# Kernel tuning notes

Hardware: AMD Instinct MI355X
Metric: run time of the kernel (lower is better)

The kernel has to match this reference:

```python
import jax, jax.numpy as jnp
import numpy as np

B, P, IN_DIM, OUT_DIM = 4, 120000, 4, 64
SPATIAL = (480, 360, 32)
EPS = 1e-5
SLOPE = 0.01  # LeakyReLU default negative slope


def setup_inputs() -> dict:
    key = jax.random.key(0)
    ks = jax.random.split(key, 10)
    pc = jax.random.normal(ks[0], (B, P, IN_DIM), dtype=jnp.float32)
    pc_indices = jax.random.randint(ks[1], (B, P, 3), 0, 32, dtype=jnp.int32)
    W1 = jax.random.normal(ks[2], (IN_DIM, 16), dtype=jnp.float32) * (1.0 / np.sqrt(IN_DIM))
    b1 = jax.random.normal(ks[3], (16,), dtype=jnp.float32) * 0.01
    g1 = jnp.ones((16,), jnp.float32)
    be1 = jnp.zeros((16,), jnp.float32)
    W2 = jax.random.normal(ks[4], (16, OUT_DIM), dtype=jnp.float32) * 0.25
    b2 = jax.random.normal(ks[5], (OUT_DIM,), dtype=jnp.float32) * 0.01
    g2 = jnp.ones((OUT_DIM,), jnp.float32)
    be2 = jnp.zeros((OUT_DIM,), jnp.float32)
    return {"pc": pc, "pc_indices": pc_indices, "W1": W1, "b1": b1, "g1": g1,
            "be1": be1, "W2": W2, "b2": b2, "g2": g2, "be2": be2}


def _bn_lrelu(h, g, b):
    # BatchNorm1d in training mode: batch mean / biased variance over points
    mean = jnp.mean(h, axis=0)
    var = jnp.mean((h - mean) ** 2, axis=0)
    h = (h - mean) / jnp.sqrt(var + EPS) * g + b
    return jnp.where(h >= 0, h, SLOPE * h)


def reference(pc, pc_indices, W1, b1, g1, be1, W2, b2, g2, be2):
    N = B * P
    x = pc.reshape(N, IN_DIM)
    bid = jnp.repeat(jnp.arange(B, dtype=jnp.int32), P)  # batch id padded in front
    coords = jnp.concatenate([bid[:, None], pc_indices.reshape(N, 3)], axis=1)  # [N,4]

    # small MLP (shuffle/recover in the original is a mathematical no-op for outputs)
    h = _bn_lrelu(x @ W1 + b1, g1, be1)
    feat = _bn_lrelu(h @ W2 + b2, g2, be2)  # [N, OUT_DIM]

    # torch.unique(dim=0) == lexicographic sort of linearized voxel keys
    S0, S1, S2 = SPATIAL
    key = (((coords[:, 0] * S0 + coords[:, 1]) * S1 + coords[:, 2]) * S2 + coords[:, 3])
    order = jnp.argsort(key)
    sk = key[order]
    is_first = jnp.concatenate([jnp.ones((1,), bool), sk[1:] != sk[:-1]])
    seg_sorted = (jnp.cumsum(is_first) - 1).astype(jnp.int32)  # segment id per sorted point
    inv = jnp.zeros((N,), jnp.int32).at[order].set(seg_sorted)  # inverse index (unsorted)

    # scatter_max into (padded, fixed-shape) voxel feature table
    voxel_feat = jax.ops.segment_max(feat, inv, num_segments=N)  # [N, OUT_DIM]
    n_uni = seg_sorted[-1] + 1
    valid = jnp.arange(N) < n_uni
    voxel_feat = jnp.where(valid[:, None], voxel_feat, 0.0)
    voxel_ind = jnp.zeros((N, 4), jnp.int32).at[seg_sorted].set(coords[order])

    return voxel_feat, voxel_ind, feat
```

## Files before the change

### kernel.cpp

```cpp
#include <hip/hip_runtime.h>

typedef unsigned int u32;
typedef unsigned char u8;

#define N_PTS 480000
#define PPB   120000
#define NKEY  131072
#define NBLK_A 256
#define NBLK_B 512
#define NT64   7500
#define SLOPE 0.01f

__device__ __forceinline__ u32 mapf(float f) {
    u32 u = __float_as_uint(f);
    return (u & 0x80000000u) ? ~u : (u | 0x80000000u);
}
__device__ __forceinline__ float unmapf(u32 m) {
    u32 u = (m & 0x80000000u) ? (m ^ 0x80000000u) : ~m;
    return __uint_as_float(u);
}

__global__ __launch_bounds__(256) void kA(const float* __restrict__ pc,
                                          const int* __restrict__ pidx,
                                          u32* __restrict__ keys,
                                          u8* __restrict__ occ,
                                          float* __restrict__ pA) {
    int t = threadIdx.x;
    float a[14];
#pragma unroll
    for (int j = 0; j < 14; ++j) a[j] = 0.f;

    for (int n = blockIdx.x * 256 + t; n < N_PTS; n += gridDim.x * 256) {
        float4 x = ((const float4*)pc)[n];
        a[0] += x.x; a[1] += x.y; a[2] += x.z; a[3] += x.w;
        a[4] += x.x * x.x; a[5] += x.x * x.y; a[6]  += x.x * x.z; a[7]  += x.x * x.w;
        a[8] += x.y * x.y; a[9] += x.y * x.z; a[10] += x.y * x.w;
        a[11] += x.z * x.z; a[12] += x.z * x.w; a[13] += x.w * x.w;

        int i0 = pidx[3 * n], i1 = pidx[3 * n + 1], i2 = pidx[3 * n + 2];
        int bid = n / PPB;
        u32 key = (u32)(bid * 32768 + i0 * 1024 + i1 * 32 + i2);
        keys[n] = key;
        occ[key] = (u8)1;
    }

    __shared__ float red[256];
    for (int j = 0; j < 14; ++j) {
        red[t] = a[j];
        __syncthreads();
        for (int s = 128; s > 0; s >>= 1) {
            if (t < s) red[t] += red[t + s];
            __syncthreads();
        }
        if (t == 0) pA[blockIdx.x * 14 + j] = red[0];
        __syncthreads();
    }
}

__global__ __launch_bounds__(64) void kR1(const float* __restrict__ pA,
                                          const float* __restrict__ W1,
                                          const float* __restrict__ b1,
                                          const float* __restrict__ g1,
                                          const float* __restrict__ be1,
                                          float* __restrict__ stats1) {
    __shared__ double S[14];
    int t = threadIdx.x;
    if (t < 14) {
        double s = 0.0;
        for (int b = 0; b < NBLK_A; ++b) s += pA[b * 14 + t];
        S[t] = s;
    }
    __syncthreads();
    if (t < 16) {
        int c = t;
        double w[4];
#pragma unroll
        for (int i = 0; i < 4; ++i) w[i] = W1[i * 16 + c];
        double sx[4] = { S[0], S[1], S[2], S[3] };
        auto sxx = [&](int i, int j) -> double {
            if (i > j) { int k = i; i = j; j = k; }
            int base = (i == 0) ? 4 : (i == 1) ? 8 : (i == 2) ? 11 : 13;
            return S[base + (j - i)];
        };
        double su = 0.0;
        for (int i = 0; i < 4; ++i) su += sx[i] * w[i];
        double q = 0.0;
        for (int i = 0; i < 4; ++i)
            for (int j = 0; j < 4; ++j) q += w[i] * w[j] * sxx(i, j);
        double b = (double)b1[c];
        double sum   = su + b * (double)N_PTS;
        double sumsq = q + 2.0 * b * su + (double)N_PTS * b * b;
        double mean = sum / (double)N_PTS;
        double var  = sumsq / (double)N_PTS - mean * mean;
        float inv = rsqrtf((float)(var + 1e-5));
        float sc = g1[c] * inv;
        stats1[c]      = sc;
        stats1[16 + c] = be1[c] - (float)mean * sc;
    }
}

__global__ __launch_bounds__(256) void kB(const float* __restrict__ pc,
                                          const float* __restrict__ W1,
                                          const float* __restrict__ b1,
                                          const float* __restrict__ stats1,
                                          const float* __restrict__ W2,
                                          const float* __restrict__ b2,
                                          float* __restrict__ pB) {
    int t = threadIdx.x;
    __shared__ float shx[256];
    __shared__ float shh[64][16];

    int c1 = t & 15;
    float w1c[4];
#pragma unroll
    for (int i = 0; i < 4; ++i) w1c[i] = W1[i * 16 + c1];
    float b1c = b1[c1], sc1 = stats1[c1], sf1 = stats1[16 + c1];

    int c2 = t & 63;
    float w2c[16];
#pragma unroll
    for (int k = 0; k < 16; ++k) w2c[k] = W2[k * 64 + c2];
    float b2c = b2[c2];
    int p0 = t >> 4;
    int pg = t >> 6;

    float accf = 0.f, accf2 = 0.f;
    for (int tile = blockIdx.x; tile < NT64; tile += gridDim.x) {
        int base = tile * 64;
        shx[t] = pc[base * 4 + t];
        __syncthreads();
#pragma unroll
        for (int i = 0; i < 4; ++i) {
            int p = p0 + 16 * i;
            float hp = b1c + shx[p * 4 + 0] * w1c[0] + shx[p * 4 + 1] * w1c[1]
                           + shx[p * 4 + 2] * w1c[2] + shx[p * 4 + 3] * w1c[3];
            float z = hp * sc1 + sf1;
            shh[p][c1] = (z >= 0.f) ? z : SLOPE * z;
        }
        __syncthreads();
#pragma unroll
        for (int j = 0; j < 16; ++j) {
            int p = pg + 4 * j;
            float f = b2c;
#pragma unroll
            for (int k = 0; k < 16; ++k) f += shh[p][k] * w2c[k];
            accf += f;
            accf2 += f * f;
        }
        __syncthreads();
    }

    __shared__ float r1[256], r2[256];
    r1[t] = accf; r2[t] = accf2;
    __syncthreads();
    if (t < 64) {
        float s1 = r1[t] + r1[t + 64] + r1[t + 128] + r1[t + 192];
        float s2 = r2[t] + r2[t + 64] + r2[t + 128] + r2[t + 192];
        pB[blockIdx.x * 128 + t]      = s1;
        pB[blockIdx.x * 128 + 64 + t] = s2;
    }
}

__global__ __launch_bounds__(64) void kR2(const float* __restrict__ pB,
                                          const float* __restrict__ g2,
                                          const float* __restrict__ be2,
                                          float* __restrict__ stats2) {
    int c = threadIdx.x;
    double sf = 0.0, sf2 = 0.0;
    for (int b = 0; b < NBLK_B; ++b) {
        sf  += pB[b * 128 + c];
        sf2 += pB[b * 128 + 64 + c];
    }
    double mean = sf / (double)N_PTS;
    double var  = sf2 / (double)N_PTS - mean * mean;
    float inv = rsqrtf((float)(var + 1e-5));
    float sc = g2[c] * inv;
    stats2[c]      = sc;
    stats2[64 + c] = be2[c] - (float)mean * sc;
}

__global__ __launch_bounds__(256) void kS1(const u32* __restrict__ occ32,
                                           u32* __restrict__ bs) {
    int t = threadIdx.x, b = blockIdx.x;
    u32 v = occ32[b * 256 + t];
    u32 c = __popc(v);
    __shared__ u32 red[256];
    red[t] = c;
    __syncthreads();
    for (int s = 128; s > 0; s >>= 1) {
        if (t < s) red[t] += red[t + s];
        __syncthreads();
    }
    if (t == 0) bs[b] = red[0];
}

__global__ __launch_bounds__(256) void kS2(const u32* __restrict__ occ32,
                                           const u32* __restrict__ bs,
                                           u32* __restrict__ rank_,
                                           u32* __restrict__ nuni) {
    int t = threadIdx.x, b = blockIdx.x;
    __shared__ u32 sbs[128];
    __shared__ u32 sexcl;
    if (t < 128) sbs[t] = bs[t];
    __syncthreads();
    if (t == 0) {
        u32 s = 0;
        for (int i = 0; i < b; ++i) s += sbs[i];
        sexcl = s;
    }
    u32 v = occ32[b * 256 + t];
    u32 c = __popc(v);
    __shared__ u32 sc[256];
    sc[t] = c;
    __syncthreads();
    for (int d = 1; d < 256; d <<= 1) {
        u32 x = (t >= d) ? sc[t - d] : 0u;
        __syncthreads();
        sc[t] += x;
        __syncthreads();
    }
    u32 run = sexcl + sc[t] - c;
    int base = b * 1024 + t * 4;
#pragma unroll
    for (int j = 0; j < 4; ++j) {
        rank_[base + j] = run;
        run += (v >> (8 * j)) & 0xffu;
    }
    if (b == 127 && t == 255) nuni[0] = run;
}

__global__ __launch_bounds__(256) void kC(const float* __restrict__ pc,
                                          const u32* __restrict__ keys,
                                          const u32* __restrict__ rank_,
                                          const float* __restrict__ W1,
                                          const float* __restrict__ b1,
                                          const float* __restrict__ stats1,
                                          const float* __restrict__ W2,
                                          const float* __restrict__ b2,
                                          const float* __restrict__ stats2,
                                          float* __restrict__ feat_out,
                                          u32* __restrict__ vf_u) {
    int t = threadIdx.x;
    __shared__ float shx[256];
    __shared__ float shh[64][16];
    __shared__ u32 shr[64];

    int c1 = t & 15;
    float w1c[4];
#pragma unroll
    for (int i = 0; i < 4; ++i) w1c[i] = W1[i * 16 + c1];
    float b1c = b1[c1], sc1 = stats1[c1], sf1 = stats1[16 + c1];

    int c2 = t & 63;
    float w2c[16];
#pragma unroll
    for (int k = 0; k < 16; ++k) w2c[k] = W2[k * 64 + c2];
    float b2c = b2[c2], sc2 = stats2[c2], sf2 = stats2[64 + c2];
    int p0 = t >> 4;
    int pg = t >> 6;

    for (int tile = blockIdx.x; tile < NT64; tile += gridDim.x) {
        int base = tile * 64;
        shx[t] = pc[base * 4 + t];
        if (t < 64) shr[t] = rank_[keys[base + t]];
        __syncthreads();
#pragma unroll
        for (int i = 0; i < 4; ++i) {
            int p = p0 + 16 * i;
            float hp = b1c + shx[p * 4 + 0] * w1c[0] + shx[p * 4 + 1] * w1c[1]
                           + shx[p * 4 + 2] * w1c[2] + shx[p * 4 + 3] * w1c[3];
            float z = hp * sc1 + sf1;
            shh[p][c1] = (z >= 0.f) ? z : SLOPE * z;
        }
        __syncthreads();
#pragma unroll
        for (int j = 0; j < 16; ++j) {
            int p = pg + 4 * j;
            float f = b2c;
#pragma unroll
            for (int k = 0; k < 16; ++k) f += shh[p][k] * w2c[k];
            float z = f * sc2 + sf2;
            float ff = (z >= 0.f) ? z : SLOPE * z;
            feat_out[(size_t)(base + p) * 64 + c2] = ff;
            atomicMax(&vf_u[(size_t)shr[p] * 64 + c2], mapf(ff));
        }
        __syncthreads();
    }
}

__global__ __launch_bounds__(256) void kD(float* __restrict__ vf,
                                          float* __restrict__ vi,
                                          const u32* __restrict__ nuni) {
    size_t i4 = (size_t)blockIdx.x * 256 + threadIdx.x;
    u32 nu = *nuni;
    if (i4 < 7680000) {
        u32 row = (u32)(i4 >> 4);
        float4* p = (float4*)vf + i4;
        float4 o;
        if (row < nu) {
            uint4 m = *(const uint4*)p;
            o.x = unmapf(m.x); o.y = unmapf(m.y); o.z = unmapf(m.z); o.w = unmapf(m.w);
        } else {
            o.x = 0.f; o.y = 0.f; o.z = 0.f; o.w = 0.f;
        }
        *p = o;
    } else {
        size_t q = i4 - 7680000;
        if (q >= nu) {
            float4 z; z.x = 0.f; z.y = 0.f; z.z = 0.f; z.w = 0.f;
            ((float4*)vi)[q] = z;
        }
    }
}

__global__ __launch_bounds__(256) void kE(const u8* __restrict__ occ,
                                          const u32* __restrict__ rank_,
                                          float* __restrict__ vi) {
    int c = blockIdx.x * 256 + threadIdx.x;
    if (occ[c]) {
        u32 r = rank_[c];
        float4 o;
        o.x = (float)(c >> 15);
        o.y = (float)((c >> 10) & 31);
        o.z = (float)((c >> 5) & 31);
        o.w = (float)(c & 31);
        ((float4*)vi)[r] = o;
    }
}

extern "C" void kernel_launch(void* const* d_in, const int* in_sizes, int n_in,
                              void* d_out, int out_size, void* d_ws, size_t ws_size,
                              hipStream_t stream) {
    const float* pc   = (const float*)d_in[0];
    const int*   pidx = (const int*)d_in[1];
    const float* W1   = (const float*)d_in[2];
    const float* b1   = (const float*)d_in[3];
    const float* g1   = (const float*)d_in[4];
    const float* be1  = (const float*)d_in[5];
    const float* W2   = (const float*)d_in[6];
    const float* b2   = (const float*)d_in[7];
    const float* g2   = (const float*)d_in[8];
    const float* be2  = (const float*)d_in[9];

    float* vf   = (float*)d_out;
    float* vi   = vf + (size_t)N_PTS * 64;
    float* feat = vi + (size_t)N_PTS * 4;

    u32* ws    = (u32*)d_ws;
    u32* keys  = ws;
    u8*  occ8  = (u8*)(ws + 480000);
    u32* occ32 = ws + 480000;
    u32* rank_ = ws + 512768;
    u32* bs    = ws + 643840;
    u32* nuni  = ws + 643968;
    float* pA     = (float*)(ws + 643984);
    float* stats1 = (float*)(ws + 647568);
    float* pB     = (float*)(ws + 647600);
    float* stats2 = (float*)(ws + 713136);

    hipMemsetAsync(occ8, 0, (size_t)NKEY, stream);
    hipMemsetAsync(vf, 0, (size_t)NKEY * 64 * 4, stream);

    kA<<<NBLK_A, 256, 0, stream>>>(pc, pidx, keys, occ8, pA);
    kR1<<<1, 64, 0, stream>>>(pA, W1, b1, g1, be1, stats1);
    kB<<<NBLK_B, 256, 0, stream>>>(pc, W1, b1, stats1, W2, b2, pB);
    kR2<<<1, 64, 0, stream>>>(pB, g2, be2, stats2);
    kS1<<<128, 256, 0, stream>>>(occ32, bs);
    kS2<<<128, 256, 0, stream>>>(occ32, bs, rank_, nuni);
    kC<<<2048, 256, 0, stream>>>(pc, keys, rank_, W1, b1, stats1, W2, b2, stats2, feat, (u32*)vf);
    kD<<<31875, 256, 0, stream>>>(vf, vi, nuni);
    kE<<<NKEY / 256, 256, 0, stream>>>(occ8, rank_, vi);
}
```

Before: 223.8 us.

## Replace atomic scatter-max with counting-sort segment reduction and covariance-based BN2 stats

New measurement: 226.2 us. About the same (+1.1%).

```diff
diff --git a/kernel.cpp b/kernel.cpp
--- a/kernel.cpp
+++ b/kernel.cpp
@@ -1,7 +1,7 @@
 #include <hip/hip_runtime.h>
 
 typedef unsigned int u32;
-typedef unsigned char u8;
+typedef unsigned long long u64;
 
 #define N_PTS 480000
 #define PPB   120000
@@ -11,19 +11,10 @@
 #define NT64   7500
 #define SLOPE 0.01f
 
-__device__ __forceinline__ u32 mapf(float f) {
-    u32 u = __float_as_uint(f);
-    return (u & 0x80000000u) ? ~u : (u | 0x80000000u);
-}
-__device__ __forceinline__ float unmapf(u32 m) {
-    u32 u = (m & 0x80000000u) ? (m ^ 0x80000000u) : ~m;
-    return __uint_as_float(u);
-}
-
 __global__ __launch_bounds__(256) void kA(const float* __restrict__ pc,
                                           const int* __restrict__ pidx,
                                           u32* __restrict__ keys,
-                                          u8* __restrict__ occ,
+                                          u32* __restrict__ cnt,
                                           float* __restrict__ pA) {
     int t = threadIdx.x;
     float a[14];
@@ -41,7 +32,7 @@
         int bid = n / PPB;
         u32 key = (u32)(bid * 32768 + i0 * 1024 + i1 * 32 + i2);
         keys[n] = key;
-        occ[key] = (u8)1;
+        atomicAdd(&cnt[key], 1u);
     }
 
     __shared__ float red[256];
@@ -103,8 +94,6 @@
                                           const float* __restrict__ W1,
                                           const float* __restrict__ b1,
                                           const float* __restrict__ stats1,
-                                          const float* __restrict__ W2,
-                                          const float* __restrict__ b2,
                                           float* __restrict__ pB) {
     int t = threadIdx.x;
     __shared__ float shx[256];
@@ -116,134 +105,172 @@
     for (int i = 0; i < 4; ++i) w1c[i] = W1[i * 16 + c1];
     float b1c = b1[c1], sc1 = stats1[c1], sf1 = stats1[16 + c1];
 
-    int c2 = t & 63;
-    float w2c[16];
-#pragma unroll
-    for (int k = 0; k < 16; ++k) w2c[k] = W2[k * 64 + c2];
-    float b2c = b2[c2];
-    int p0 = t >> 4;
-    int pg = t >> 6;
-
-    float accf = 0.f, accf2 = 0.f;
+    int pi = 0, pj = 0;
+    if (t >= 16 && t < 152) {
+        int rem = t - 16, i = 0;
+        while (rem >= 16 - i) { rem -= 16 - i; ++i; }
+        pi = i; pj = i + rem;
+    }
+
+    float acc = 0.f;
     for (int tile = blockIdx.x; tile < NT64; tile += gridDim.x) {
         int base = tile * 64;
         shx[t] = pc[base * 4 + t];
         __syncthreads();
 #pragma unroll
         for (int i = 0; i < 4; ++i) {
-            int p = p0 + 16 * i;
+            int p = (t >> 4) + 16 * i;
             float hp = b1c + shx[p * 4 + 0] * w1c[0] + shx[p * 4 + 1] * w1c[1]
                            + shx[p * 4 + 2] * w1c[2] + shx[p * 4 + 3] * w1c[3];
             float z = hp * sc1 + sf1;
             shh[p][c1] = (z >= 0.f) ? z : SLOPE * z;
         }
         __syncthreads();
-#pragma unroll
-        for (int j = 0; j < 16; ++j) {
-            int p = pg + 4 * j;
-            float f = b2c;
-#pragma unroll
-            for (int k = 0; k < 16; ++k) f += shh[p][k] * w2c[k];
-            accf += f;
-            accf2 += f * f;
-        }
-        __syncthreads();
-    }
-
-    __shared__ float r1[256], r2[256];
-    r1[t] = accf; r2[t] = accf2;
+        if (t < 16) {
+#pragma unroll 4
+            for (int p = 0; p < 64; ++p) acc += shh[p][t];
+        } else if (t < 152) {
+#pragma unroll 4
+            for (int p = 0; p < 64; ++p) acc += shh[p][pi] * shh[p][pj];
+        }
+        __syncthreads();
+    }
+    if (t < 152) pB[blockIdx.x * 152 + t] = acc;
+}
+
+__global__ __launch_bounds__(256) void kR2(const float* __restrict__ pB,
+                                           const float* __restrict__ W2,
+                                           const float* __restrict__ b2,
+                                           const float* __restrict__ g2,
+                                           const float* __restrict__ be2,
+                                           float* __restrict__ stats2) {
+    __shared__ double S[152];
+    int t = threadIdx.x;
+    if (t < 152) {
+        double s = 0.0;
+        for (int b = 0; b < NBLK_B; ++b) s += pB[b * 152 + t];
+        S[t] = s;
+    }
     __syncthreads();
     if (t < 64) {
-        float s1 = r1[t] + r1[t + 64] + r1[t + 128] + r1[t + 192];
-        float s2 = r2[t] + r2[t + 64] + r2[t + 128] + r2[t + 192];
-        pB[blockIdx.x * 128 + t]      = s1;
-        pB[blockIdx.x * 128 + 64 + t] = s2;
-    }
-}
-
-__global__ __launch_bounds__(64) void kR2(const float* __restrict__ pB,
-                                          const float* __restrict__ g2,
-                                          const float* __restrict__ be2,
-                                          float* __restrict__ stats2) {
-    int c = threadIdx.x;
-    double sf = 0.0, sf2 = 0.0;
-    for (int b = 0; b < NBLK_B; ++b) {
-        sf  += pB[b * 128 + c];
-        sf2 += pB[b * 128 + 64 + c];
-    }
-    double mean = sf / (double)N_PTS;
-    double var  = sf2 / (double)N_PTS - mean * mean;
-    float inv = rsqrtf((float)(var + 1e-5));
-    float sc = g2[c] * inv;
-    stats2[c]      = sc;
-    stats2[64 + c] = be2[c] - (float)mean * sc;
-}
-
-__global__ __launch_bounds__(256) void kS1(const u32* __restrict__ occ32,
-                                           u32* __restrict__ bs) {
+        double w[16];
+#pragma unroll
+        for (int k = 0; k < 16; ++k) w[k] = W2[k * 64 + t];
+        double sh = 0.0;
+        for (int k = 0; k < 16; ++k) sh += w[k] * S[k];
+        auto qidx = [&](int i, int j) { return 16 + i * 16 - (i * (i - 1)) / 2 + (j - i); };
+        double q = 0.0;
+        for (int i = 0; i < 16; ++i) {
+            q += w[i] * w[i] * S[qidx(i, i)];
+            double t2 = 0.0;
+            for (int j = i + 1; j < 16; ++j) t2 += w[j] * S[qidx(i, j)];
+            q += 2.0 * w[i] * t2;
+        }
+        double b = (double)b2[t];
+        double sum   = sh + b * (double)N_PTS;
+        double sumsq = q + 2.0 * b * sh + (double)N_PTS * b * b;
+        double mean = sum / (double)N_PTS;
+        double var  = sumsq / (double)N_PTS - mean * mean;
+        float inv = rsqrtf((float)(var + 1e-5));
+        float sc = g2[t] * inv;
+        stats2[t]      = sc;
+        stats2[64 + t] = be2[t] - (float)mean * sc;
+    }
+}
+
+__global__ __launch_bounds__(256) void kS1(const u32* __restrict__ cnt,
+                                           u32* __restrict__ bsum) {
     int t = threadIdx.x, b = blockIdx.x;
-    u32 v = occ32[b * 256 + t];
-    u32 c = __popc(v);
-    __shared__ u32 red[256];
-    red[t] = c;
+    uint4 c4 = ((const uint4*)cnt)[b * 256 + t];
+    u32 cs = c4.x + c4.y + c4.z + c4.w;
+    u32 os = (c4.x > 0) + (c4.y > 0) + (c4.z > 0) + (c4.w > 0);
+    __shared__ u32 rc[256], ro[256];
+    rc[t] = cs; ro[t] = os;
     __syncthreads();
     for (int s = 128; s > 0; s >>= 1) {
-        if (t < s) red[t] += red[t + s];
-        __syncthreads();
-    }
-    if (t == 0) bs[b] = red[0];
-}
-
-__global__ __launch_bounds__(256) void kS2(const u32* __restrict__ occ32,
-                                           const u32* __restrict__ bs,
-                                           u32* __restrict__ rank_,
+        if (t < s) { rc[t] += rc[t + s]; ro[t] += ro[t + s]; }
+        __syncthreads();
+    }
+    if (t == 0) { bsum[2 * b] = rc[0]; bsum[2 * b + 1] = ro[0]; }
+}
+
+__global__ __launch_bounds__(256) void kS2(u32* __restrict__ cnt,
+                                           const u32* __restrict__ bsum,
+                                           u32* __restrict__ startc,
+                                           float* __restrict__ vi,
                                            u32* __restrict__ nuni) {
     int t = threadIdx.x, b = blockIdx.x;
-    __shared__ u32 sbs[128];
-    __shared__ u32 sexcl;
-    if (t < 128) sbs[t] = bs[t];
+    __shared__ u32 sbc[128], sbo[128];
+    __shared__ u32 cOff, oOff;
+    __shared__ u64 scan[256];
+    if (t < 128) { sbc[t] = bsum[2 * t]; sbo[t] = bsum[2 * t + 1]; }
+
+    uint4 c4 = ((const uint4*)cnt)[b * 256 + t];
+    u32 cv[4] = { c4.x, c4.y, c4.z, c4.w };
+    u32 cs = cv[0] + cv[1] + cv[2] + cv[3];
+    u32 os = (cv[0] > 0) + (cv[1] > 0) + (cv[2] > 0) + (cv[3] > 0);
+    scan[t] = ((u64)cs << 32) | (u64)os;
     __syncthreads();
     if (t == 0) {
-        u32 s = 0;
-        for (int i = 0; i < b; ++i) s += sbs[i];
-        sexcl = s;
-    }
-    u32 v = occ32[b * 256 + t];
-    u32 c = __popc(v);
-    __shared__ u32 sc[256];
-    sc[t] = c;
-    __syncthreads();
+        u32 a = 0, o = 0;
+        for (int i = 0; i < b; ++i) { a += sbc[i]; o += sbo[i]; }
+        cOff = a; oOff = o;
+    }
     for (int d = 1; d < 256; d <<= 1) {
-        u32 x = (t >= d) ? sc[t - d] : 0u;
-        __syncthreads();
-        sc[t] += x;
-        __syncthreads();
-    }
-    u32 run = sexcl + sc[t] - c;
-    int base = b * 1024 + t * 4;
+        u64 v = (t >= d) ? scan[t - d] : 0ull;
+        __syncthreads();
+        scan[t] += v;
+        __syncthreads();
+    }
+    u64 ex = scan[t] - (((u64)cs << 32) | (u64)os);
+    u32 start = cOff + (u32)(ex >> 32);
+    u32 rank  = oOff + (u32)(ex & 0xffffffffull);
+
+    int kbase = b * 1024 + t * 4;
 #pragma unroll
     for (int j = 0; j < 4; ++j) {
-        rank_[base + j] = run;
-        run += (v >> (8 * j)) & 0xffu;
-    }
-    if (b == 127 && t == 255) nuni[0] = run;
+        u32 k = (u32)(kbase + j);
+        cnt[k] = start;
+        if (cv[j] > 0) {
+            startc[rank] = start;
+            float4 o;
+            o.x = (float)(k >> 15);
+            o.y = (float)((k >> 10) & 31);
+            o.z = (float)((k >> 5) & 31);
+            o.w = (float)(k & 31);
+            ((float4*)vi)[rank] = o;
+            rank++;
+        }
+        start += cv[j];
+    }
+    if (b == 127 && t == 255) {
+        nuni[0] = rank;
+        startc[rank] = N_PTS;
+    }
+}
+
+__global__ __launch_bounds__(256) void kP(const u32* __restrict__ keys,
+                                          u32* __restrict__ cursor,
+                                          u32* __restrict__ pid) {
+    int n = blockIdx.x * 256 + threadIdx.x;
+    if (n < N_PTS) {
+        u32 k = keys[n];
+        u32 pos = atomicAdd(&cursor[k], 1u);
+        pid[pos] = (u32)n;
+    }
 }
 
 __global__ __launch_bounds__(256) void kC(const float* __restrict__ pc,
-                                          const u32* __restrict__ keys,
-                                          const u32* __restrict__ rank_,
                                           const float* __restrict__ W1,
                                           const float* __restrict__ b1,
                                           const float* __restrict__ stats1,
                                           const float* __restrict__ W2,
                                           const float* __restrict__ b2,
                                           const float* __restrict__ stats2,
-                                          float* __restrict__ feat_out,
-                                          u32* __restrict__ vf_u) {
+                                          float* __restrict__ feat_out) {
     int t = threadIdx.x;
     __shared__ float shx[256];
     __shared__ float shh[64][16];
-    __shared__ u32 shr[64];
 
     int c1 = t & 15;
     float w1c[4];
@@ -256,17 +283,15 @@
 #pragma unroll
     for (int k = 0; k < 16; ++k) w2c[k] = W2[k * 64 + c2];
     float b2c = b2[c2], sc2 = stats2[c2], sf2 = stats2[64 + c2];
-    int p0 = t >> 4;
     int pg = t >> 6;
 
     for (int tile = blockIdx.x; tile < NT64; tile += gridDim.x) {
         int base = tile * 64;
         shx[t] = pc[base * 4 + t];
-        if (t < 64) shr[t] = rank_[keys[base + t]];
         __syncthreads();
 #pragma unroll
         for (int i = 0; i < 4; ++i) {
-            int p = p0 + 16 * i;
+            int p = (t >> 4) + 16 * i;
             float hp = b1c + shx[p * 4 + 0] * w1c[0] + shx[p * 4 + 1] * w1c[1]
                            + shx[p * 4 + 2] * w1c[2] + shx[p * 4 + 3] * w1c[3];
             float z = hp * sc1 + sf1;
@@ -282,49 +307,37 @@
             float z = f * sc2 + sf2;
             float ff = (z >= 0.f) ? z : SLOPE * z;
             feat_out[(size_t)(base + p) * 64 + c2] = ff;
-            atomicMax(&vf_u[(size_t)shr[p] * 64 + c2], mapf(ff));
-        }
-        __syncthreads();
-    }
-}
-
-__global__ __launch_bounds__(256) void kD(float* __restrict__ vf,
-                                          float* __restrict__ vi,
-                                          const u32* __restrict__ nuni) {
-    size_t i4 = (size_t)blockIdx.x * 256 + threadIdx.x;
+        }
+        __syncthreads();
+    }
+}
+
+__global__ __launch_bounds__(256) void kV(const float* __restrict__ feat,
+                                          const u32* __restrict__ pid,
+                                          const u32* __restrict__ startc,
+                                          const u32* __restrict__ nuni,
+                                          float* __restrict__ vf,
+                                          float* __restrict__ vi) {
     u32 nu = *nuni;
-    if (i4 < 7680000) {
-        u32 row = (u32)(i4 >> 4);
-        float4* p = (float4*)vf + i4;
-        float4 o;
-        if (row < nu) {
-            uint4 m = *(const uint4*)p;
-            o.x = unmapf(m.x); o.y = unmapf(m.y); o.z = unmapf(m.z); o.w = unmapf(m.w);
-        } else {
-            o.x = 0.f; o.y = 0.f; o.z = 0.f; o.w = 0.f;
-        }
-        *p = o;
+    u32 r0 = blockIdx.x * 4;
+    int w = threadIdx.x >> 6, lane = threadIdx.x & 63;
+
+    if (threadIdx.x < 16) {
+        u32 row = r0 + (threadIdx.x >> 2);
+        if (row >= nu) vi[(size_t)row * 4 + (threadIdx.x & 3)] = 0.f;
+    }
+
+    u32 r = r0 + (u32)w;
+    if (r < nu) {
+        u32 s = startc[r], e = startc[r + 1];
+        float m = -3.4e38f;
+        for (u32 i = s; i < e; ++i) {
+            u32 p = pid[i];
+            m = fmaxf(m, feat[(size_t)p * 64 + lane]);
+        }
+        vf[(size_t)r * 64 + lane] = m;
     } else {
-        size_t q = i4 - 7680000;
-        if (q >= nu) {
-            float4 z; z.x = 0.f; z.y = 0.f; z.z = 0.f; z.w = 0.f;
-            ((float4*)vi)[q] = z;
-        }
-    }
-}
-
-__global__ __launch_bounds__(256) void kE(const u8* __restrict__ occ,
-                                          const u32* __restrict__ rank_,
-                                          float* __restrict__ vi) {
-    int c = blockIdx.x * 256 + threadIdx.x;
-    if (occ[c]) {
-        u32 r = rank_[c];
-        float4 o;
-        o.x = (float)(c >> 15);
-        o.y = (float)((c >> 10) & 31);
-        o.z = (float)((c >> 5) & 31);
-        o.w = (float)(c & 31);
-        ((float4*)vi)[r] = o;
+        vf[(size_t)r * 64 + lane] = 0.f;
     }
 }
 
@@ -346,28 +359,27 @@
     float* vi   = vf + (size_t)N_PTS * 64;
     float* feat = vi + (size_t)N_PTS * 4;
 
-    u32* ws    = (u32*)d_ws;
-    u32* keys  = ws;
-    u8*  occ8  = (u8*)(ws + 480000);
-    u32* occ32 = ws + 480000;
-    u32* rank_ = ws + 512768;
-    u32* bs    = ws + 643840;
-    u32* nuni  = ws + 643968;
-    float* pA     = (float*)(ws + 643984);
-    float* stats1 = (float*)(ws + 647568);
-    float* pB     = (float*)(ws + 647600);
-    float* stats2 = (float*)(ws + 713136);
-
-    hipMemsetAsync(occ8, 0, (size_t)NKEY, stream);
-    hipMemsetAsync(vf, 0, (size_t)NKEY * 64 * 4, stream);
-
-    kA<<<NBLK_A, 256, 0, stream>>>(pc, pidx, keys, occ8, pA);
+    u32* ws     = (u32*)d_ws;
+    u32* keys   = ws;
+    u32* cnt    = ws + 480000;
+    u32* startc = ws + 611072;
+    u32* bsum   = ws + 742148;
+    u32* nuni   = ws + 742404;
+    u32* pid    = ws + 742420;
+    float* pA     = (float*)(ws + 1222420);
+    float* stats1 = (float*)(ws + 1226004);
+    float* pB     = (float*)(ws + 1226036);
+    float* stats2 = (float*)(ws + 1303860);
+
+    hipMemsetAsync(cnt, 0, (size_t)NKEY * 4, stream);
+
+    kA<<<NBLK_A, 256, 0, stream>>>(pc, pidx, keys, cnt, pA);
     kR1<<<1, 64, 0, stream>>>(pA, W1, b1, g1, be1, stats1);
-    kB<<<NBLK_B, 256, 0, stream>>>(pc, W1, b1, stats1, W2, b2, pB);
-    kR2<<<1, 64, 0, stream>>>(pB, g2, be2, stats2);
-    kS1<<<128, 256, 0, stream>>>(occ32, bs);
-    kS2<<<128, 256, 0, stream>>>(occ32, bs, rank_, nuni);
-    kC<<<2048, 256, 0, stream>>>(pc, keys, rank_, W1, b1, stats1, W2, b2, stats2, feat, (u32*)vf);
-    kD<<<31875, 256, 0, stream>>>(vf, vi, nuni);
-    kE<<<NKEY / 256, 256, 0, stream>>>(occ8, rank_, vi);
-}
+    kB<<<NBLK_B, 256, 0, stream>>>(pc, W1, b1, stats1, pB);
+    kR2<<<1, 256, 0, stream>>>(pB, W2, b2, g2, be2, stats2);
+    kS1<<<128, 256, 0, stream>>>(cnt, bsum);
+    kS2<<<128, 256, 0, stream>>>(cnt, bsum, startc, vi, nuni);
+    kP<<<1875, 256, 0, stream>>>(keys, cnt, pid);
+    kC<<<2048, 256, 0, stream>>>(pc, W1, b1, stats1, W2, b2, stats2, feat);
+    kV<<<120000, 256, 0, stream>>>(feat, pid, startc, nuni, vf, vi);
+}
```
